# Kernel optimization log

Measured on AMD Instinct MI355X. Metric: run time of the kernel, lower is better.

Reference implementation:

```python
import jax, jax.numpy as jnp
import numpy as np
import math

B, T, D = 2, 2048, 4096
H, HD = 32, 128  # n_head, head_dim; H*HD == D
THETA = 10000.0


def _rope_tables(T, hd, theta):
    # standard RoPE: freqs_i = theta^(-2i/hd), angle[t,i] = t * freqs_i
    inv = 1.0 / (theta ** (np.arange(0, hd, 2, dtype=np.float32) / hd))  # [hd/2]
    ang = np.arange(T, dtype=np.float32)[:, None] * inv[None, :]          # [T, hd/2]
    return jnp.asarray(np.cos(ang)), jnp.asarray(np.sin(ang))


def setup_inputs() -> dict:
    key = jax.random.key(0)
    ks = jax.random.split(key, 5)
    scale = 1.0 / math.sqrt(D)
    x = jax.random.normal(ks[0], (B, T, D), dtype=jnp.float32)
    Wq = jax.random.normal(ks[1], (D, H * HD), dtype=jnp.float32) * scale
    Wk = jax.random.normal(ks[2], (D, H * HD), dtype=jnp.float32) * scale
    Wv = jax.random.normal(ks[3], (D, H * HD), dtype=jnp.float32) * scale
    Wo = jax.random.normal(ks[4], (D, D), dtype=jnp.float32) * scale
    fc, fs = _rope_tables(T, HD, THETA)
    return {"x": x, "freqs_cos": fc, "freqs_sin": fs,
            "Wq": Wq, "Wk": Wk, "Wv": Wv, "Wo": Wo}


def _apply_rope(t, cos, sin):
    # t: [B, T, H, HD]; complex rotation on interleaved (even, odd) pairs
    tp = t.reshape(*t.shape[:-1], HD // 2, 2)
    xr, xi = tp[..., 0], tp[..., 1]
    c = cos[None, :, None, :]  # [1, T, 1, HD/2]
    s = sin[None, :, None, :]
    out_r = xr * c - xi * s
    out_i = xr * s + xi * c
    return jnp.stack([out_r, out_i], axis=-1).reshape(t.shape)


def reference(x, freqs_cos, freqs_sin, Wq, Wk, Wv, Wo):
    Bc, Tc, _ = x.shape
    q = (x @ Wq).reshape(Bc, Tc, H, HD)
    k = (x @ Wk).reshape(Bc, Tc, H, HD)
    v = (x @ Wv).reshape(Bc, Tc, H, HD)
    q = _apply_rope(q, freqs_cos, freqs_sin)
    k = _apply_rope(k, freqs_cos, freqs_sin)
    scale = 1.0 / math.sqrt(HD)
    scores = jnp.einsum('bqhd,bkhd->bhqk', q, k) * scale  # [B,H,T,T]
    causal = jnp.tril(jnp.ones((Tc, Tc), dtype=bool))
    scores = jnp.where(causal[None, None], scores, -jnp.inf)
    attn = jax.nn.softmax(scores, axis=-1)
    y = jnp.einsum('bhqk,bkhd->bqhd', attn, v).reshape(Bc, Tc, H * HD)
    return y @ Wo
```

## Files before the change

### kernel.cpp

```cpp
#include <hip/hip_runtime.h>

typedef unsigned short ushort_t;
typedef unsigned int uint32;

typedef float f32x4 __attribute__((ext_vector_type(4)));
typedef __bf16 bf16x8 __attribute__((ext_vector_type(8)));
typedef unsigned short us8 __attribute__((ext_vector_type(8)));
typedef unsigned short us4 __attribute__((ext_vector_type(4)));

#define TSEQ 2048
#define DMODEL 4096

__device__ __forceinline__ ushort_t f2bf(float f) {
  uint32 u = __builtin_bit_cast(uint32, f);
  u += 0x7FFFu + ((u >> 16) & 1u);
  return (ushort_t)(u >> 16);
}
__device__ __forceinline__ float bf2f(ushort_t u) {
  return __builtin_bit_cast(float, ((uint32)u) << 16);
}

__device__ __forceinline__ void gload_lds16(const void* g, void* l) {
  auto gp = (const __attribute__((address_space(1))) void*)g;
  auto lp = (__attribute__((address_space(3))) void*)l;
  __builtin_amdgcn_global_load_lds(gp, lp, 16, 0, 0);
}

__global__ __launch_bounds__(256) void k_cast_bf16(const float* __restrict__ in,
                                                   ushort_t* __restrict__ out, int n4) {
  int g = blockIdx.x * 256 + threadIdx.x;
  if (g >= n4) return;
  float4 v = *(const float4*)(in + (size_t)g * 4);
  us4 o; o[0] = f2bf(v.x); o[1] = f2bf(v.y); o[2] = f2bf(v.z); o[3] = f2bf(v.w);
  *(us4*)(out + (size_t)g * 4) = o;
}

__global__ __launch_bounds__(256) void k_transpose_cast4(const float* __restrict__ W0,
                                                         const float* __restrict__ W1,
                                                         const float* __restrict__ W2,
                                                         const float* __restrict__ W3,
                                                         ushort_t* __restrict__ WTbase) {
  __shared__ __align__(16) ushort_t ts[64 * 72];
  const float* Ws[4] = {W0, W1, W2, W3};
  const float* W = Ws[blockIdx.z];
  ushort_t* WT = WTbase + (size_t)blockIdx.z * DMODEL * DMODEL;
  const int tid = threadIdx.x;
  const int n0 = blockIdx.x * 64, k0 = blockIdx.y * 64;
  #pragma unroll
  for (int it = 0; it < 4; ++it) {
    int e = it * 256 + tid;
    int r = e >> 4, c4 = e & 15;
    float4 v = *(const float4*)(W + (size_t)(k0 + r) * DMODEL + n0 + c4 * 4);
    us4 o; o[0] = f2bf(v.x); o[1] = f2bf(v.y); o[2] = f2bf(v.z); o[3] = f2bf(v.w);
    *(us4*)&ts[r * 72 + c4 * 4] = o;
  }
  __syncthreads();
  #pragma unroll
  for (int it = 0; it < 4; ++it) {
    int e = it * 256 + tid;
    int r2 = e >> 4, c4 = e & 15;
    us4 o;
    #pragma unroll
    for (int j = 0; j < 4; ++j) o[j] = ts[(c4 * 4 + j) * 72 + r2];
    *(us4*)(WT + (size_t)(n0 + r2) * DMODEL + k0 + c4 * 4) = o;
  }
}

#define MM16(AF, BF, MO, NO)                                                     \
  _Pragma("unroll") for (int i_ = 0; i_ < 4; ++i_)                               \
  _Pragma("unroll") for (int j_ = 0; j_ < 2; ++j_)                               \
  _Pragma("unroll") for (int k_ = 0; k_ < 2; ++k_)                               \
    acc[(MO) + i_][(NO) + j_] = __builtin_amdgcn_mfma_f32_16x16x32_bf16(         \
        AF[i_][k_], BF[j_][k_], acc[(MO) + i_][(NO) + j_], 0, 0, 0);

#define LDA(DST, BASE, MO)                                                       \
  _Pragma("unroll") for (int i_ = 0; i_ < 4; ++i_) {                             \
    DST[i_][0] = *(const bf16x8*)((BASE) + ofsA0 + ((MO) + i_) * 1024);          \
    DST[i_][1] = *(const bf16x8*)((BASE) + ofsA1 + ((MO) + i_) * 1024);          \
  }
#define LDB(DST, BASE, NO)                                                       \
  _Pragma("unroll") for (int j_ = 0; j_ < 2; ++j_) {                             \
    DST[j_][0] = *(const bf16x8*)((BASE) + ofsB0 + ((NO) + j_) * 1024);          \
    DST[j_][1] = *(const bf16x8*)((BASE) + ofsB1 + ((NO) + j_) * 1024);          \
  }
#define MEMBAR() asm volatile("" ::: "memory")

template <bool OUT_BF16, bool ROPE>
__global__ __launch_bounds__(512, 2)
void k_gemm256(const ushort_t* __restrict__ A, const ushort_t* __restrict__ Bt,
               void* __restrict__ Cv, int M, int N, int K,
               const float* __restrict__ fc, const float* __restrict__ fs) {
  __shared__ __align__(16) ushort_t As[2][256 * 64];
  __shared__ __align__(16) ushort_t Bs[2][256 * 64];
  const int tid = threadIdx.x;
  const int w = tid >> 6, l = tid & 63;
  const int wr = w >> 2, wc = w & 3;
  const int lg = l >> 4, lc = l & 15;

  const int nwg = gridDim.x;
  const int cpx = nwg >> 3;
  const int wg = (blockIdx.x & 7) * cpx + (blockIdx.x >> 3);
  const int nbn = N >> 8;
  const int bm = wg / nbn, bn = wg % nbn;

  const ushort_t* Ab = A + (size_t)(bm * 256) * K;
  const ushort_t* Bb = Bt + (size_t)(bn * 256) * K;

  int aS0[2], aS1[2], bS0[2], bS1[2];
  #pragma unroll
  for (int j = 0; j < 2; ++j) {
    aS0[j] = (w < 4) ? (2 * w + j) : (8 + 2 * w + j);
    aS1[j] = aS0[j] + 8;
    int i2 = 2 * w + j;
    bS0[j] = (i2 >> 2) * 8 + (i2 & 3);
    bS1[j] = bS0[j] + 4;
  }
  const int rowoff = l >> 3;
  const int swz = (l & 7) ^ rowoff;

  const int ofsA0 = (wr * 128 + lc) * 64 + (((0 * 4 + lg) ^ (lc & 7)) * 8);
  const int ofsA1 = (wr * 128 + lc) * 64 + (((1 * 4 + lg) ^ (lc & 7)) * 8);
  const int ofsB0 = (wc * 64 + lc) * 64 + (((0 * 4 + lg) ^ (lc & 7)) * 8);
  const int ofsB1 = (wc * 64 + lc) * 64 + (((1 * 4 + lg) ^ (lc & 7)) * 8);

  f32x4 acc[8][4];
  #pragma unroll
  for (int m = 0; m < 8; ++m)
    #pragma unroll
    for (int n = 0; n < 4; ++n) acc[m][n] = (f32x4){0.f, 0.f, 0.f, 0.f};

  const int NT = K >> 6;
  auto stg = [&](const ushort_t* gb, ushort_t* lds, int s, int tl) {
    int k0 = ((tl < NT) ? tl : (NT - 1)) << 6;
    gload_lds16(gb + (size_t)(s * 8 + rowoff) * K + k0 + swz * 8, lds + s * 512);
  };

  bf16x8 aX[4][2], b0[2][2], b1[2][2];

  stg(Ab, As[0], aS0[0], 0); stg(Ab, As[0], aS0[1], 0);
  stg(Ab, As[0], aS1[0], 0); stg(Ab, As[0], aS1[1], 0);
  stg(Bb, Bs[0], bS0[0], 0); stg(Bb, Bs[0], bS0[1], 0);
  stg(Bb, Bs[0], bS1[0], 0); stg(Bb, Bs[0], bS1[1], 0);
  stg(Ab, As[1], aS0[0], 1); stg(Ab, As[1], aS0[1], 1);
  stg(Ab, As[1], aS1[0], 1); stg(Ab, As[1], aS1[1], 1);
  stg(Bb, Bs[1], bS0[0], 1); stg(Bb, Bs[1], bS0[1], 1);
  stg(Bb, Bs[1], bS1[0], 1); stg(Bb, Bs[1], bS1[1], 1);
  asm volatile("s_waitcnt vmcnt(8)" ::: "memory");
  __builtin_amdgcn_s_barrier();
  MEMBAR();
  LDA(aX, As[0], 0);
  LDB(b0, Bs[0], 0);

  auto pass = [&](ushort_t* Ac, ushort_t* Bc, const ushort_t* Ao, const ushort_t* Bo, int t) {
    LDB(b1, Bc, 2);
    __builtin_amdgcn_s_setprio(1);
    MM16(aX, b0, 0, 0);
    __builtin_amdgcn_s_setprio(0);
    MEMBAR(); __builtin_amdgcn_s_barrier(); MEMBAR();
    stg(Ab, Ac, aS0[0], t + 2); stg(Ab, Ac, aS0[1], t + 2);
    stg(Bb, Bc, bS0[0], t + 2); stg(Bb, Bc, bS0[1], t + 2);
    __builtin_amdgcn_s_setprio(1);
    MM16(aX, b1, 0, 2);
    __builtin_amdgcn_s_setprio(0);
    LDA(aX, Ac, 4);
    MEMBAR(); __builtin_amdgcn_s_barrier(); MEMBAR();
    stg(Bb, Bc, bS1[0], t + 2); stg(Bb, Bc, bS1[1], t + 2);
    __builtin_amdgcn_s_setprio(1);
    MM16(aX, b1, 4, 2);
    __builtin_amdgcn_s_setprio(0);
    asm volatile("s_waitcnt vmcnt(6)" ::: "memory");
    MEMBAR(); __builtin_amdgcn_s_barrier(); MEMBAR();
    stg(Ab, Ac, aS1[0], t + 2); stg(Ab, Ac, aS1[1], t + 2);
    __builtin_amdgcn_s_setprio(1);
    MM16(aX, b0, 4, 0);
    __builtin_amdgcn_s_setprio(0);
    if (t + 1 < NT) {
      LDA(aX, Ao, 0);
      LDB(b0, Bo, 0);
    }
    MEMBAR(); __builtin_amdgcn_s_barrier(); MEMBAR();
  };

  for (int t = 0; t < NT; t += 2) {
    pass(As[0], Bs[0], As[1], Bs[1], t);
    pass(As[1], Bs[1], As[0], Bs[0], t + 1);
  }

  #pragma unroll
  for (int m = 0; m < 8; ++m) {
    int row0 = bm * 256 + wr * 128 + m * 16 + lg * 4;
    #pragma unroll
    for (int n = 0; n < 4; ++n) {
      int col = bn * 256 + wc * 64 + n * 16 + lc;
      if (ROPE) {
        int i0 = (col & 127) >> 1;
        #pragma unroll
        for (int r = 0; r < 4; ++r) {
          int tt = (row0 + r) & (TSEQ - 1);
          float c = fc[tt * 64 + i0];
          float s = fs[tt * 64 + i0];
          float v = acc[m][n][r];
          float p = __shfl_xor(v, 1);
          float ov = (lc & 1) ? (p * s + v * c) : (v * c - p * s);
          ((ushort_t*)Cv)[(size_t)(row0 + r) * N + col] = f2bf(ov);
        }
      } else {
        #pragma unroll
        for (int r = 0; r < 4; ++r) {
          float v = acc[m][n][r];
          if (OUT_BF16) ((ushort_t*)Cv)[(size_t)(row0 + r) * N + col] = f2bf(v);
          else          ((float*)Cv)[(size_t)(row0 + r) * N + col] = v;
        }
      }
    }
  }
}

__global__ __launch_bounds__(512, 2)
void k_attn(const ushort_t* __restrict__ QK, const ushort_t* __restrict__ Vt,
            ushort_t* __restrict__ Y) {
  __shared__ __align__(16) ushort_t Ks[2][64 * 128];
  __shared__ __align__(16) ushort_t Vs[2][128 * 64];
  __shared__ __align__(16) ushort_t Ps[8][16 * 64];
  const int id = blockIdx.x;
  const int xcd = id & 7, slot = id >> 3;
  const int bx = slot & 7, gHi = slot >> 3;
  const int g = gHi * 8 + xcd;
  const int h = g & 31, b = g >> 5;
  const int tid = threadIdx.x;
  const int w = tid >> 6, l = tid & 63;
  const int lg = l >> 4, lc = l & 15;
  const float scale = 0.08838834764831845f;
  const float THR = 8.0f;
  const int QKS = 8192;

  auto stageKV = [&](int kv0, int buf) {
    #pragma unroll
    for (int i = 0; i < 2; ++i) {
      int seg = w * 2 + i;
      {
        int row = seg * 4 + (l >> 4);
        int csrc = (l & 15) ^ (row & 7);
        gload_lds16(QK + (size_t)(b * TSEQ + kv0 + row) * QKS + 4096 + h * 128 + csrc * 8,
                    &Ks[buf][seg * 512]);
      }
      {
        int row = seg * 8 + (l >> 3);
        int csrc = (l & 7) ^ (l >> 3);
        gload_lds16(Vt + (size_t)(h * 128 + row) * DMODEL + b * TSEQ + kv0 + csrc * 8,
                    &Vs[buf][seg * 512]);
      }
    }
  };

  for (int qi = 0; qi < 2; ++qi) {
    const int qt = qi ? (15 - bx) : bx;
    const int q0 = qt * 128;
    const int wrow0 = q0 + w * 16;

    bf16x8 qf[4];
    {
      const ushort_t* qp = QK + (size_t)(b * TSEQ + wrow0 + lc) * QKS + h * 128;
      #pragma unroll
      for (int ks = 0; ks < 4; ++ks) qf[ks] = *(const bf16x8*)(qp + ks * 32 + lg * 8);
    }

    float m_r[4], lp[4];
    #pragma unroll
    for (int r = 0; r < 4; ++r) { m_r[r] = -1e30f; lp[r] = 0.f; }
    f32x4 o[8];
    #pragma unroll
    for (int t = 0; t < 8; ++t) o[t] = (f32x4){0.f, 0.f, 0.f, 0.f};

    const int nkv = (qt + 1) * 2;
    stageKV(0, 0);
    for (int kt = 0; kt < nkv; ++kt) {
      const int cur = kt & 1;
      const int kv0 = kt * 64;
      if (kt + 1 < nkv) {
        stageKV((kt + 1) * 64, cur ^ 1);
        asm volatile("s_waitcnt vmcnt(4)" ::: "memory");
      } else {
        asm volatile("s_waitcnt vmcnt(0)" ::: "memory");
      }
      __builtin_amdgcn_s_barrier();

      if (kv0 <= wrow0 + 15) {
        f32x4 s[4];
        __builtin_amdgcn_s_setprio(1);
        #pragma unroll
        for (int n = 0; n < 4; ++n) {
          s[n] = (f32x4){0.f, 0.f, 0.f, 0.f};
          #pragma unroll
          for (int ks = 0; ks < 4; ++ks) {
            int row = n * 16 + lc;
            bf16x8 kf = *(const bf16x8*)&Ks[cur][row * 128 + ((ks * 32 + lg * 8) ^ ((row & 7) * 8))];
            s[n] = __builtin_amdgcn_mfma_f32_16x16x32_bf16(qf[ks], kf, s[n], 0, 0, 0);
          }
        }
        __builtin_amdgcn_s_setprio(0);

        float sv[4][4];
        if (kv0 + 63 > wrow0) {
          #pragma unroll
          for (int n = 0; n < 4; ++n)
            #pragma unroll
            for (int r = 0; r < 4; ++r) {
              float x = s[n][r] * scale;
              int kvg = kv0 + n * 16 + lc;
              int qg = wrow0 + lg * 4 + r;
              sv[n][r] = (kvg > qg) ? -1e30f : x;
            }
        } else {
          #pragma unroll
          for (int n = 0; n < 4; ++n)
            #pragma unroll
            for (int r = 0; r < 4; ++r) sv[n][r] = s[n][r] * scale;
        }

        float pmax[4];
        #pragma unroll
        for (int r = 0; r < 4; ++r)
          pmax[r] = fmaxf(fmaxf(sv[0][r], sv[1][r]), fmaxf(sv[2][r], sv[3][r]));
        bool ok = (pmax[0] <= m_r[0] + THR) && (pmax[1] <= m_r[1] + THR) &&
                  (pmax[2] <= m_r[2] + THR) && (pmax[3] <= m_r[3] + THR);
        if (!__all(ok)) {
          #pragma unroll
          for (int r = 0; r < 4; ++r) {
            float mx = pmax[r];
            #pragma unroll
            for (int off = 1; off < 16; off <<= 1) mx = fmaxf(mx, __shfl_xor(mx, off, 16));
            float mn = fmaxf(m_r[r], mx);
            float al = __expf(m_r[r] - mn);
            m_r[r] = mn;
            lp[r] *= al;
            #pragma unroll
            for (int t = 0; t < 8; ++t) o[t][r] *= al;
          }
        }

        #pragma unroll
        for (int n = 0; n < 4; ++n)
          #pragma unroll
          for (int r = 0; r < 4; ++r) {
            float p = __expf(sv[n][r] - m_r[r]);
            lp[r] += p;
            int row = lg * 4 + r, col = n * 16 + lc;
            Ps[w][row * 64 + (col ^ (lg * 16))] = f2bf(p);
          }

        __builtin_amdgcn_s_setprio(1);
        #pragma unroll
        for (int kvs = 0; kvs < 2; ++kvs) {
          bf16x8 pa = *(const bf16x8*)&Ps[w][lc * 64 + ((kvs * 32 + lg * 8) ^ ((lc >> 2) * 16))];
          #pragma unroll
          for (int t = 0; t < 8; ++t) {
            int vrow = t * 16 + lc;
            bf16x8 vb = *(const bf16x8*)&Vs[cur][vrow * 64 + ((kvs * 32 + lg * 8) ^ ((vrow & 7) * 8))];
            o[t] = __builtin_amdgcn_mfma_f32_16x16x32_bf16(pa, vb, o[t], 0, 0, 0);
          }
        }
        __builtin_amdgcn_s_setprio(0);
      }
      asm volatile("" ::: "memory");
      __builtin_amdgcn_s_barrier();
    }

    float linv[4];
    #pragma unroll
    for (int r = 0; r < 4; ++r) {
      float ls = lp[r];
      #pragma unroll
      for (int off = 1; off < 16; off <<= 1) ls += __shfl_xor(ls, off, 16);
      linv[r] = 1.0f / ls;
    }

    #pragma unroll
    for (int t = 0; t < 8; ++t)
      #pragma unroll
      for (int r = 0; r < 4; ++r) {
        int row = wrow0 + lg * 4 + r;
        int col = h * 128 + t * 16 + lc;
        Y[(size_t)(b * TSEQ + row) * DMODEL + col] = f2bf(o[t][r] * linv[r]);
      }
  }
}

extern "C" void kernel_launch(void* const* d_in, const int* in_sizes, int n_in,
                              void* d_out, int out_size, void* d_ws, size_t ws_size,
                              hipStream_t stream) {
  const float* x  = (const float*)d_in[0];
  const float* fc = (const float*)d_in[1];
  const float* fs = (const float*)d_in[2];
  const float* Wq = (const float*)d_in[3];
  const float* Wk = (const float*)d_in[4];
  const float* Wv = (const float*)d_in[5];
  const float* Wo = (const float*)d_in[6];

  const size_t SZ = (size_t)4096 * 4096;
  ushort_t* xb  = (ushort_t*)d_ws;
  ushort_t* WqT = xb + SZ;
  ushort_t* WkT = WqT + SZ;
  ushort_t* WvT = WkT + SZ;
  ushort_t* WoT = WvT + SZ;
  ushort_t* qk  = WoT + SZ;
  ushort_t* vT  = qk + 2 * SZ;
  ushort_t* yb  = vT + SZ;

  k_cast_bf16<<<16384, 256, 0, stream>>>(x, xb, 4194304);
  dim3 tg(64, 64, 4);
  k_transpose_cast4<<<tg, 256, 0, stream>>>(Wq, Wk, Wv, Wo, WqT);

  k_gemm256<true, true><<<512, 512, 0, stream>>>(xb, WqT, qk, 4096, 8192, 4096, fc, fs);
  k_gemm256<true, false><<<256, 512, 0, stream>>>(WvT, xb, vT, 4096, 4096, 4096, nullptr, nullptr);

  k_attn<<<512, 512, 0, stream>>>(qk, vT, yb);

  k_gemm256<false, false><<<256, 512, 0, stream>>>(yb, WoT, d_out, 4096, 4096, 4096, nullptr, nullptr);
}
```

Measured before the change: 864.0 us.

## Replace 256-tile pipelined GEMM with simple single-buffered 128-tile GEMM

Replaces the 256x256 double-buffered, barrier-interleaved GEMM (512 threads, BK=64) with a 128x128 tile, 256-thread kernel. The new kernel uses BK=32, a single LDS buffer and waits on vmcnt(0) every iteration. This gives more workgroups and lower LDS use per block for higher occupancy. It loses the overlap of global loads with MFMA work and halves data reuse per tile.

```diff
diff --git a/kernel.cpp b/kernel.cpp
--- a/kernel.cpp
+++ b/kernel.cpp
@@ -66,132 +66,83 @@
   }
 }
 
-#define MM16(AF, BF, MO, NO)                                                     \
-  _Pragma("unroll") for (int i_ = 0; i_ < 4; ++i_)                               \
-  _Pragma("unroll") for (int j_ = 0; j_ < 2; ++j_)                               \
-  _Pragma("unroll") for (int k_ = 0; k_ < 2; ++k_)                               \
-    acc[(MO) + i_][(NO) + j_] = __builtin_amdgcn_mfma_f32_16x16x32_bf16(         \
-        AF[i_][k_], BF[j_][k_], acc[(MO) + i_][(NO) + j_], 0, 0, 0);
-
-#define LDA(DST, BASE, MO)                                                       \
-  _Pragma("unroll") for (int i_ = 0; i_ < 4; ++i_) {                             \
-    DST[i_][0] = *(const bf16x8*)((BASE) + ofsA0 + ((MO) + i_) * 1024);          \
-    DST[i_][1] = *(const bf16x8*)((BASE) + ofsA1 + ((MO) + i_) * 1024);          \
-  }
-#define LDB(DST, BASE, NO)                                                       \
-  _Pragma("unroll") for (int j_ = 0; j_ < 2; ++j_) {                             \
-    DST[j_][0] = *(const bf16x8*)((BASE) + ofsB0 + ((NO) + j_) * 1024);          \
-    DST[j_][1] = *(const bf16x8*)((BASE) + ofsB1 + ((NO) + j_) * 1024);          \
-  }
-#define MEMBAR() asm volatile("" ::: "memory")
-
 template <bool OUT_BF16, bool ROPE>
-__global__ __launch_bounds__(512, 2)
-void k_gemm256(const ushort_t* __restrict__ A, const ushort_t* __restrict__ Bt,
+__global__ __launch_bounds__(256, 3)
+void k_gemm128(const ushort_t* __restrict__ A, const ushort_t* __restrict__ Bt,
                void* __restrict__ Cv, int M, int N, int K,
                const float* __restrict__ fc, const float* __restrict__ fs) {
-  __shared__ __align__(16) ushort_t As[2][256 * 64];
-  __shared__ __align__(16) ushort_t Bs[2][256 * 64];
+  __shared__ __align__(16) ushort_t As[128 * 32];
+  __shared__ __align__(16) ushort_t Bs[128 * 32];
   const int tid = threadIdx.x;
   const int w = tid >> 6, l = tid & 63;
-  const int wr = w >> 2, wc = w & 3;
+  const int wm = w >> 1, wn = w & 1;
   const int lg = l >> 4, lc = l & 15;
 
   const int nwg = gridDim.x;
   const int cpx = nwg >> 3;
   const int wg = (blockIdx.x & 7) * cpx + (blockIdx.x >> 3);
-  const int nbn = N >> 8;
+  const int nbn = N >> 7;
   const int bm = wg / nbn, bn = wg % nbn;
 
-  const ushort_t* Ab = A + (size_t)(bm * 256) * K;
-  const ushort_t* Bb = Bt + (size_t)(bn * 256) * K;
-
-  int aS0[2], aS1[2], bS0[2], bS1[2];
+  const ushort_t* Ab = A + (size_t)(bm * 128) * K;
+  const ushort_t* Bb = Bt + (size_t)(bn * 128) * K;
+
+  const int csrc = (l & 3) ^ ((l >> 3) & 3);
+  const ushort_t* gA[2]; const ushort_t* gB[2];
+  int dstOff[2];
   #pragma unroll
   for (int j = 0; j < 2; ++j) {
-    aS0[j] = (w < 4) ? (2 * w + j) : (8 + 2 * w + j);
-    aS1[j] = aS0[j] + 8;
-    int i2 = 2 * w + j;
-    bS0[j] = (i2 >> 2) * 8 + (i2 & 3);
-    bS1[j] = bS0[j] + 4;
-  }
-  const int rowoff = l >> 3;
-  const int swz = (l & 7) ^ rowoff;
-
-  const int ofsA0 = (wr * 128 + lc) * 64 + (((0 * 4 + lg) ^ (lc & 7)) * 8);
-  const int ofsA1 = (wr * 128 + lc) * 64 + (((1 * 4 + lg) ^ (lc & 7)) * 8);
-  const int ofsB0 = (wc * 64 + lc) * 64 + (((0 * 4 + lg) ^ (lc & 7)) * 8);
-  const int ofsB1 = (wc * 64 + lc) * 64 + (((1 * 4 + lg) ^ (lc & 7)) * 8);
-
-  f32x4 acc[8][4];
-  #pragma unroll
-  for (int m = 0; m < 8; ++m)
+    int row = w * 32 + j * 16 + (l >> 2);
+    gA[j] = Ab + (size_t)row * K + csrc * 8;
+    gB[j] = Bb + (size_t)row * K + csrc * 8;
+    dstOff[j] = (w * 32 + j * 16) * 32;
+  }
+
+  int offA[4], offB[4];
+  #pragma unroll
+  for (int m = 0; m < 4; ++m)
+    offA[m] = (wm * 64 + m * 16 + lc) * 32 + ((lg ^ ((lc >> 1) & 3)) * 8);
+  #pragma unroll
+  for (int n = 0; n < 4; ++n)
+    offB[n] = (wn * 64 + n * 16 + lc) * 32 + ((lg ^ ((lc >> 1) & 3)) * 8);
+
+  f32x4 acc[4][4];
+  #pragma unroll
+  for (int m = 0; m < 4; ++m)
     #pragma unroll
     for (int n = 0; n < 4; ++n) acc[m][n] = (f32x4){0.f, 0.f, 0.f, 0.f};
 
-  const int NT = K >> 6;
-  auto stg = [&](const ushort_t* gb, ushort_t* lds, int s, int tl) {
-    int k0 = ((tl < NT) ? tl : (NT - 1)) << 6;
-    gload_lds16(gb + (size_t)(s * 8 + rowoff) * K + k0 + swz * 8, lds + s * 512);
-  };
-
-  bf16x8 aX[4][2], b0[2][2], b1[2][2];
-
-  stg(Ab, As[0], aS0[0], 0); stg(Ab, As[0], aS0[1], 0);
-  stg(Ab, As[0], aS1[0], 0); stg(Ab, As[0], aS1[1], 0);
-  stg(Bb, Bs[0], bS0[0], 0); stg(Bb, Bs[0], bS0[1], 0);
-  stg(Bb, Bs[0], bS1[0], 0); stg(Bb, Bs[0], bS1[1], 0);
-  stg(Ab, As[1], aS0[0], 1); stg(Ab, As[1], aS0[1], 1);
-  stg(Ab, As[1], aS1[0], 1); stg(Ab, As[1], aS1[1], 1);
-  stg(Bb, Bs[1], bS0[0], 1); stg(Bb, Bs[1], bS0[1], 1);
-  stg(Bb, Bs[1], bS1[0], 1); stg(Bb, Bs[1], bS1[1], 1);
-  asm volatile("s_waitcnt vmcnt(8)" ::: "memory");
-  __builtin_amdgcn_s_barrier();
-  MEMBAR();
-  LDA(aX, As[0], 0);
-  LDB(b0, Bs[0], 0);
-
-  auto pass = [&](ushort_t* Ac, ushort_t* Bc, const ushort_t* Ao, const ushort_t* Bo, int t) {
-    LDB(b1, Bc, 2);
+  const int NT = K >> 5;
+  for (int t = 0; t < NT; ++t) {
+    const int k0 = t << 5;
+    __syncthreads();
+    gload_lds16(gA[0] + k0, &As[dstOff[0]]);
+    gload_lds16(gA[1] + k0, &As[dstOff[1]]);
+    gload_lds16(gB[0] + k0, &Bs[dstOff[0]]);
+    gload_lds16(gB[1] + k0, &Bs[dstOff[1]]);
+    asm volatile("s_waitcnt vmcnt(0)" ::: "memory");
+    __syncthreads();
+
+    bf16x8 af[4], bfv[4];
+    #pragma unroll
+    for (int m = 0; m < 4; ++m) af[m] = *(const bf16x8*)&As[offA[m]];
+    #pragma unroll
+    for (int n = 0; n < 4; ++n) bfv[n] = *(const bf16x8*)&Bs[offB[n]];
     __builtin_amdgcn_s_setprio(1);
-    MM16(aX, b0, 0, 0);
+    #pragma unroll
+    for (int m = 0; m < 4; ++m)
+      #pragma unroll
+      for (int n = 0; n < 4; ++n)
+        acc[m][n] = __builtin_amdgcn_mfma_f32_16x16x32_bf16(af[m], bfv[n], acc[m][n], 0, 0, 0);
     __builtin_amdgcn_s_setprio(0);
-    MEMBAR(); __builtin_amdgcn_s_barrier(); MEMBAR();
-    stg(Ab, Ac, aS0[0], t + 2); stg(Ab, Ac, aS0[1], t + 2);
-    stg(Bb, Bc, bS0[0], t + 2); stg(Bb, Bc, bS0[1], t + 2);
-    __builtin_amdgcn_s_setprio(1);
-    MM16(aX, b1, 0, 2);
-    __builtin_amdgcn_s_setprio(0);
-    LDA(aX, Ac, 4);
-    MEMBAR(); __builtin_amdgcn_s_barrier(); MEMBAR();
-    stg(Bb, Bc, bS1[0], t + 2); stg(Bb, Bc, bS1[1], t + 2);
-    __builtin_amdgcn_s_setprio(1);
-    MM16(aX, b1, 4, 2);
-    __builtin_amdgcn_s_setprio(0);
-    asm volatile("s_waitcnt vmcnt(6)" ::: "memory");
-    MEMBAR(); __builtin_amdgcn_s_barrier(); MEMBAR();
-    stg(Ab, Ac, aS1[0], t + 2); stg(Ab, Ac, aS1[1], t + 2);
-    __builtin_amdgcn_s_setprio(1);
-    MM16(aX, b0, 4, 0);
-    __builtin_amdgcn_s_setprio(0);
-    if (t + 1 < NT) {
-      LDA(aX, Ao, 0);
-      LDB(b0, Bo, 0);
-    }
-    MEMBAR(); __builtin_amdgcn_s_barrier(); MEMBAR();
-  };
-
-  for (int t = 0; t < NT; t += 2) {
-    pass(As[0], Bs[0], As[1], Bs[1], t);
-    pass(As[1], Bs[1], As[0], Bs[0], t + 1);
-  }
-
-  #pragma unroll
-  for (int m = 0; m < 8; ++m) {
-    int row0 = bm * 256 + wr * 128 + m * 16 + lg * 4;
+  }
+
+  #pragma unroll
+  for (int m = 0; m < 4; ++m) {
+    int row0 = bm * 128 + wm * 64 + m * 16 + lg * 4;
     #pragma unroll
     for (int n = 0; n < 4; ++n) {
-      int col = bn * 256 + wc * 64 + n * 16 + lc;
+      int col = bn * 128 + wn * 64 + n * 16 + lc;
       if (ROPE) {
         int i0 = (col & 127) >> 1;
         #pragma unroll
@@ -411,10 +362,10 @@
   dim3 tg(64, 64, 4);
   k_transpose_cast4<<<tg, 256, 0, stream>>>(Wq, Wk, Wv, Wo, WqT);
 
-  k_gemm256<true, true><<<512, 512, 0, stream>>>(xb, WqT, qk, 4096, 8192, 4096, fc, fs);
-  k_gemm256<true, false><<<256, 512, 0, stream>>>(WvT, xb, vT, 4096, 4096, 4096, nullptr, nullptr);
+  k_gemm128<true, true><<<2048, 256, 0, stream>>>(xb, WqT, qk, 4096, 8192, 4096, fc, fs);
+  k_gemm128<true, false><<<1024, 256, 0, stream>>>(WvT, xb, vT, 4096, 4096, 4096, nullptr, nullptr);
 
   k_attn<<<512, 512, 0, stream>>>(qk, vT, yb);
 
-  k_gemm256<false, false><<<256, 512, 0, stream>>>(yb, WoT, d_out, 4096, 4096, 4096, nullptr, nullptr);
-}
+  k_gemm128<false, false><<<1024, 256, 0, stream>>>(yb, WoT, d_out, 4096, 4096, 4096, nullptr, nullptr);
+}
```

After: 914.5 us. +5.8%, slower.
